# Optimization experiments

Measured on AMD Instinct MI355X. Metric: run time of the kernel, lower is better.

The kernel has to match this reference:

```python
import jax, jax.numpy as jnp
import numpy as np

N = 1048576          # total points
B = 2048             # number of point clouds (segments)
FEAT = 64            # per-point feature dim
ENC = 32             # neighborhood encoder output dim
RADIUS = 1.0


def _linear_params(key, fan_in, fan_out):
    k1, k2 = jax.random.split(key)
    bound = 1.0 / np.sqrt(fan_in)
    w = jax.random.uniform(k1, (fan_in, fan_out), minval=-bound, maxval=bound, dtype=jnp.float32)
    b = jax.random.uniform(k2, (fan_out,), minval=-bound, maxval=bound, dtype=jnp.float32)
    return w, b


def setup_inputs() -> dict:
    key = jax.random.key(0)
    ks = jax.random.split(key, 10)
    points = jax.random.normal(ks[0], (N, 3), dtype=jnp.float32)
    features = jax.random.normal(ks[1], (N, FEAT), dtype=jnp.float32)
    batch = jnp.sort(jax.random.randint(ks[2], (N,), 0, B)).astype(jnp.int64)
    w_ne, b_ne = _linear_params(ks[3], 3, ENC)
    w1, b1 = _linear_params(ks[4], ENC + FEAT, 128)
    w2, b2 = _linear_params(ks[5], 128, 128)
    w3, b3 = _linear_params(ks[6], 128, 128)
    wg1, bg1 = _linear_params(ks[7], 128, 128)
    wg2, bg2 = _linear_params(ks[8], 128, 64)
    wg3, bg3 = _linear_params(ks[9], 64, 32)
    return {"points": points, "features": features, "batch": batch,
            "w_ne": w_ne, "b_ne": b_ne,
            "w1": w1, "b1": b1, "w2": w2, "b2": b2, "w3": w3, "b3": b3,
            "wg1": wg1, "bg1": bg1, "wg2": wg2, "bg2": bg2, "wg3": wg3, "bg3": bg3}


def _segment_max(x, batch, num_segments):
    pooled = jax.ops.segment_max(x, batch, num_segments=num_segments, indices_are_sorted=True)
    # guard empty segments (segment_max fills with -inf)
    return jnp.where(jnp.isneginf(pooled), 0.0, pooled)


def reference(points, features, batch, w_ne, b_ne, w1, b1, w2, b2, w3, b3,
              wg1, bg1, wg2, bg2, wg3, bg3):
    relative_points = points / RADIUS                       # [N, 3]
    # neighborhood encoder: per-point Linear+ReLU, then segment max-pool -> [B, ENC]
    enc = jax.nn.relu(relative_points @ w_ne + b_ne)        # [N, ENC]
    rel_encoded = _segment_max(enc, batch, B)               # [B, ENC]
    rel_enc_mapped = rel_encoded[batch]                     # gather -> [N, ENC]
    fc_input = jnp.concatenate([rel_enc_mapped, features], axis=1)  # [N, ENC+FEAT]
    h = jax.nn.relu(fc_input @ w1 + b1)                     # [N, 128]
    h = jax.nn.relu(h @ w2 + b2)                            # [N, 128]
    h = jax.nn.relu(h @ w3 + b3)                            # [N, 128]
    pooled = _segment_max(h, batch, B)                      # [B, 128]
    g = jax.nn.relu(pooled @ wg1 + bg1)                     # [B, 128]
    g = jax.nn.relu(g @ wg2 + bg2)                          # [B, 64]
    g = jax.nn.relu(g @ wg3 + bg3)                          # [B, 32]
    return g
```

## Files before the change

kernel.cpp:

```cpp
#include <hip/hip_runtime.h>
#include <hip/hip_fp16.h>

#define N_PTS 1048576
#define BSEG  2048
#define XSTR  72

typedef _Float16 half8  __attribute__((ext_vector_type(8)));
typedef _Float16 half4  __attribute__((ext_vector_type(4)));
typedef float    floatx4 __attribute__((ext_vector_type(4)));

__global__ __launch_bounds__(256) void wconv(const float* __restrict__ w1,
                                             const float* __restrict__ w2,
                                             const float* __restrict__ w3,
                                             _Float16* __restrict__ w1T,
                                             _Float16* __restrict__ w2T,
                                             _Float16* __restrict__ w3T) {
    int idx = blockIdx.x * 256 + threadIdx.x;
    if (idx < 8192) {
        int j = idx >> 6, k = idx & 63;
        w1T[idx] = (_Float16)w1[(32 + k) * 128 + j];
    } else if (idx < 8192 + 16384) {
        int i = idx - 8192; int j = i >> 7, k = i & 127;
        w2T[i] = (_Float16)w2[k * 128 + j];
    } else if (idx < 8192 + 32768) {
        int i = idx - 8192 - 16384; int j = i >> 7, k = i & 127;
        w3T[i] = (_Float16)w3[k * 128 + j];
    }
}

__global__ __launch_bounds__(256) void enc_pool(const float* __restrict__ pts,
                                                const int* __restrict__ batch,
                                                const float* __restrict__ wne,
                                                const float* __restrict__ bne,
                                                const float* __restrict__ w1,
                                                const float* __restrict__ b1,
                                                float* __restrict__ b1p) {
    const int b = blockIdx.x, tid = threadIdx.x;
    __shared__ float swne[96];
    __shared__ float sbne[32];
    __shared__ float red[4][32];
    __shared__ float sEnc[32];
    if (tid < 96) swne[tid] = wne[tid];
    if (tid < 32) sbne[tid] = bne[tid];

    int lo = 0, hi = N_PTS;
    while (lo < hi) { int mid = (lo + hi) >> 1; if (batch[mid] < b) lo = mid + 1; else hi = mid; }
    const int start = lo;
    hi = N_PTS;
    while (lo < hi) { int mid = (lo + hi) >> 1; if (batch[mid] < b + 1) lo = mid + 1; else hi = mid; }
    const int end = lo;
    __syncthreads();

    float mx[32];
#pragma unroll
    for (int j = 0; j < 32; j++) mx[j] = 0.f;
    for (int p = start + tid; p < end; p += 256) {
        float x0 = pts[3 * p], x1 = pts[3 * p + 1], x2 = pts[3 * p + 2];
#pragma unroll
        for (int j = 0; j < 32; j++) {
            float e = fmaf(x0, swne[j], fmaf(x1, swne[32 + j], fmaf(x2, swne[64 + j], sbne[j])));
            mx[j] = fmaxf(mx[j], e);
        }
    }
#pragma unroll
    for (int j = 0; j < 32; j++) {
#pragma unroll
        for (int off = 1; off < 64; off <<= 1)
            mx[j] = fmaxf(mx[j], __shfl_xor(mx[j], off, 64));
    }
    const int wv = tid >> 6;
    if ((tid & 63) == 0) {
#pragma unroll
        for (int j = 0; j < 32; j++) red[wv][j] = mx[j];
    }
    __syncthreads();
    if (tid < 32)
        sEnc[tid] = fmaxf(fmaxf(red[0][tid], red[1][tid]), fmaxf(red[2][tid], red[3][tid]));
    __syncthreads();
    if (tid < 128) {
        float acc = b1[tid];
#pragma unroll 8
        for (int k = 0; k < 32; k++) acc = fmaf(sEnc[k], w1[k * 128 + tid], acc);
        b1p[b * 128 + tid] = acc;
    }
}

__global__ __launch_bounds__(256, 3) void fused_mlp(
    const float* __restrict__ feat, const int* __restrict__ batch,
    const float* __restrict__ b1p_g,
    const _Float16* __restrict__ w1T, const _Float16* __restrict__ w2T,
    const _Float16* __restrict__ w3T,
    const float* __restrict__ b2, const float* __restrict__ b3,
    const float* __restrict__ wg1, const float* __restrict__ bg1,
    const float* __restrict__ wg2, const float* __restrict__ bg2,
    const float* __restrict__ wg3, const float* __restrict__ bg3,
    float* __restrict__ out) {
    __shared__ __attribute__((aligned(16))) _Float16 xf[3][16 * XSTR];
    __shared__ __attribute__((aligned(16))) _Float16 h1s[2][16 * 128];
    __shared__ __attribute__((aligned(16))) _Float16 h2s[2][16 * 128];
    __shared__ float pooled[128];
    __shared__ float g1s[128];
    __shared__ float g2s[64];

    const int b = blockIdx.x, tid = threadIdx.x;
    const int lane = tid & 63, jq = tid >> 6;
    const int l15 = lane & 15, quad = lane >> 4;

    int lo = 0, hi = N_PTS;
    while (lo < hi) { int mid = (lo + hi) >> 1; if (batch[mid] < b) lo = mid + 1; else hi = mid; }
    const int start = lo;
    hi = N_PTS;
    while (lo < hi) { int mid = (lo + hi) >> 1; if (batch[mid] < b + 1) lo = mid + 1; else hi = mid; }
    const int end = lo;
    const int n = end - start;
    const int niter = (n + 15) >> 4;

    const int jc0 = jq * 32 + l15, jc1 = jc0 + 16;
    half8 w1f[2][2], w2f[2][4], w3f[2][4];
#pragma unroll
    for (int ks = 0; ks < 2; ks++) {
        w1f[0][ks] = *(const half8*)(w1T + jc0 * 64 + ks * 32 + quad * 8);
        w1f[1][ks] = *(const half8*)(w1T + jc1 * 64 + ks * 32 + quad * 8);
    }
#pragma unroll
    for (int ks = 0; ks < 4; ks++) {
        w2f[0][ks] = *(const half8*)(w2T + jc0 * 128 + ks * 32 + quad * 8);
        w2f[1][ks] = *(const half8*)(w2T + jc1 * 128 + ks * 32 + quad * 8);
        w3f[0][ks] = *(const half8*)(w3T + jc0 * 128 + ks * 32 + quad * 8);
        w3f[1][ks] = *(const half8*)(w3T + jc1 * 128 + ks * 32 + quad * 8);
    }
    float bb1[2], bb2[2], bb3[2];
    bb1[0] = b1p_g[b * 128 + jc0]; bb1[1] = b1p_g[b * 128 + jc1];
    bb2[0] = b2[jc0]; bb2[1] = b2[jc1];
    bb3[0] = b3[jc0]; bb3[1] = b3[jc1];

    const int srow = tid >> 4, scol = tid & 15;
    floatx4 pf;
    auto issue = [&](int it) {
        int p = start + it * 16 + srow;
        if (p < end) pf = *(const floatx4*)(feat + (size_t)p * 64 + scol * 4);
        else         pf = (floatx4){0.f, 0.f, 0.f, 0.f};
    };
    auto commitSlot = [&](int slot) {
        half4 hv = {(_Float16)pf.x, (_Float16)pf.y, (_Float16)pf.z, (_Float16)pf.w};
        *(half4*)(&xf[slot][srow * XSTR + scol * 4]) = hv;
    };
    auto storeH = [&](_Float16* hbuf, floatx4* acc, float* bb) {
#pragma unroll
        for (int jt = 0; jt < 2; jt++) {
            int c = jq * 32 + jt * 16 + l15;
#pragma unroll
            for (int r = 0; r < 4; r++) {
                int rr = quad * 4 + r;
                float v = fmaxf(acc[jt][r] + bb[jt], 0.f);
                hbuf[rr * 128 + ((((c >> 3) ^ rr) & 15) << 3) + (c & 7)] = (_Float16)v;
            }
        }
    };

    if (niter > 0) { issue(0); commitSlot(0); if (niter > 1) issue(1); }
    __syncthreads();

    float vmax[2] = {0.f, 0.f};

    for (int it = 0; it < niter + 2; ++it) {
        const bool doL1 = (it < niter);
        const bool doL2 = (it >= 1) && (it <= niter);
        const bool doL3 = (it >= 2);

        half8 a3[4], a2[4], a1[2];
        if (doL3) {
            const _Float16* src = h2s[(it - 2) & 1];
#pragma unroll
            for (int ks = 0; ks < 4; ks++)
                a3[ks] = *(const half8*)(&src[(l15 << 7) + ((((ks * 4 + quad) ^ l15) & 15) << 3)]);
        }
        if (doL2) {
            const _Float16* src = h1s[(it - 1) & 1];
#pragma unroll
            for (int ks = 0; ks < 4; ks++)
                a2[ks] = *(const half8*)(&src[(l15 << 7) + ((((ks * 4 + quad) ^ l15) & 15) << 3)]);
        }
        if (doL1) {
            const _Float16* src = xf[it % 3];
#pragma unroll
            for (int ks = 0; ks < 2; ks++)
                a1[ks] = *(const half8*)(&src[l15 * XSTR + ks * 32 + quad * 8]);
        }
        if (it + 1 < niter) commitSlot((it + 1) % 3);
        if (it + 2 < niter) issue(it + 2);

        if (doL3) {
            floatx4 acc[2];
            acc[0] = (floatx4){0.f, 0.f, 0.f, 0.f};
            acc[1] = (floatx4){0.f, 0.f, 0.f, 0.f};
#pragma unroll
            for (int ks = 0; ks < 4; ks++) {
                acc[0] = __builtin_amdgcn_mfma_f32_16x16x32_f16(a3[ks], w3f[0][ks], acc[0], 0, 0, 0);
                acc[1] = __builtin_amdgcn_mfma_f32_16x16x32_f16(a3[ks], w3f[1][ks], acc[1], 0, 0, 0);
            }
            const int rowbase = (it - 2) * 16 + quad * 4;
#pragma unroll
            for (int jt = 0; jt < 2; jt++) {
#pragma unroll
                for (int r = 0; r < 4; r++) {
                    float v = ((rowbase + r) < n) ? fmaxf(acc[jt][r] + bb3[jt], 0.f) : 0.f;
                    vmax[jt] = fmaxf(vmax[jt], v);
                }
            }
        }
        if (doL2) {
            floatx4 acc[2];
            acc[0] = (floatx4){0.f, 0.f, 0.f, 0.f};
            acc[1] = (floatx4){0.f, 0.f, 0.f, 0.f};
#pragma unroll
            for (int ks = 0; ks < 4; ks++) {
                acc[0] = __builtin_amdgcn_mfma_f32_16x16x32_f16(a2[ks], w2f[0][ks], acc[0], 0, 0, 0);
                acc[1] = __builtin_amdgcn_mfma_f32_16x16x32_f16(a2[ks], w2f[1][ks], acc[1], 0, 0, 0);
            }
            storeH(h2s[(it - 1) & 1], acc, bb2);
        }
        if (doL1) {
            floatx4 acc[2];
            acc[0] = (floatx4){0.f, 0.f, 0.f, 0.f};
            acc[1] = (floatx4){0.f, 0.f, 0.f, 0.f};
#pragma unroll
            for (int ks = 0; ks < 2; ks++) {
                acc[0] = __builtin_amdgcn_mfma_f32_16x16x32_f16(a1[ks], w1f[0][ks], acc[0], 0, 0, 0);
                acc[1] = __builtin_amdgcn_mfma_f32_16x16x32_f16(a1[ks], w1f[1][ks], acc[1], 0, 0, 0);
            }
            storeH(h1s[it & 1], acc, bb1);
        }
        __syncthreads();
    }

#pragma unroll
    for (int jt = 0; jt < 2; jt++) {
        float m = vmax[jt];
        m = fmaxf(m, __shfl_xor(m, 16, 64));
        m = fmaxf(m, __shfl_xor(m, 32, 64));
        if (quad == 0) pooled[jq * 32 + jt * 16 + l15] = m;
    }
    __syncthreads();

    if (tid < 128) {
        float acc = bg1[tid];
#pragma unroll 8
        for (int k = 0; k < 128; k++) acc = fmaf(pooled[k], wg1[k * 128 + tid], acc);
        g1s[tid] = fmaxf(acc, 0.f);
    }
    __syncthreads();
    if (tid < 64) {
        float acc = bg2[tid];
#pragma unroll 8
        for (int k = 0; k < 128; k++) acc = fmaf(g1s[k], wg2[k * 64 + tid], acc);
        g2s[tid] = fmaxf(acc, 0.f);
    }
    __syncthreads();
    if (tid < 32) {
        float acc = bg3[tid];
#pragma unroll 8
        for (int k = 0; k < 64; k++) acc = fmaf(g2s[k], wg3[k * 32 + tid], acc);
        out[b * 32 + tid] = fmaxf(acc, 0.f);
    }
}

extern "C" void kernel_launch(void* const* d_in, const int* in_sizes, int n_in,
                              void* d_out, int out_size, void* d_ws, size_t ws_size,
                              hipStream_t stream) {
    const float* points = (const float*)d_in[0];
    const float* feat   = (const float*)d_in[1];
    const int*   batch  = (const int*)d_in[2];
    const float* w_ne   = (const float*)d_in[3];
    const float* b_ne   = (const float*)d_in[4];
    const float* w1  = (const float*)d_in[5];
    const float* b1  = (const float*)d_in[6];
    const float* w2  = (const float*)d_in[7];
    const float* b2  = (const float*)d_in[8];
    const float* w3  = (const float*)d_in[9];
    const float* b3  = (const float*)d_in[10];
    const float* wg1 = (const float*)d_in[11];
    const float* bg1 = (const float*)d_in[12];
    const float* wg2 = (const float*)d_in[13];
    const float* bg2 = (const float*)d_in[14];
    const float* wg3 = (const float*)d_in[15];
    const float* bg3 = (const float*)d_in[16];
    float* out = (float*)d_out;

    char* ws = (char*)d_ws;
    float*    b1p = (float*)ws;
    _Float16* w1T = (_Float16*)(ws + 1048576);
    _Float16* w2T = (_Float16*)(ws + 1048576 + 16384);
    _Float16* w3T = (_Float16*)(ws + 1048576 + 16384 + 32768);

    wconv<<<160, 256, 0, stream>>>(w1, w2, w3, w1T, w2T, w3T);
    enc_pool<<<BSEG, 256, 0, stream>>>(points, batch, w_ne, b_ne, w1, b1, b1p);
    fused_mlp<<<BSEG, 256, 0, stream>>>(feat, batch, b1p, w1T, w2T, w3T,
                                        b2, b3, wg1, bg1, wg2, bg2, wg3, bg3, out);
}
```

Baseline: 567.8 us.

## Tile MLP over fixed 256-row blocks with atomic segment-max pooling

The fused MLP stops assigning one block per segment. Each block now takes a fixed 256-point tile and processes 64-row chunks through three MFMA layers. Segment max-pooling goes through integer atomicMax, first into a shared-memory slot table and then into a global pooled buffer; the head MLP moves to a separate kernel. The encoder output is no longer folded into a per-segment bias: it is gathered per row and concatenated as 32 extra K columns of layer 1. The aim is to remove load imbalance from variable segment sizes and the per-block binary search. The cost is a memset, atomics, an extra kernel launch and extra layer-1 work.

```diff
diff --git a/kernel.cpp b/kernel.cpp
--- a/kernel.cpp
+++ b/kernel.cpp
@@ -3,11 +3,13 @@
 
 #define N_PTS 1048576
 #define BSEG  2048
-#define XSTR  72
+#define XSTR  104
+#define NSLOT 8
 
 typedef _Float16 half8  __attribute__((ext_vector_type(8)));
 typedef _Float16 half4  __attribute__((ext_vector_type(4)));
 typedef float    floatx4 __attribute__((ext_vector_type(4)));
+typedef int      intx4   __attribute__((ext_vector_type(4)));
 
 __global__ __launch_bounds__(256) void wconv(const float* __restrict__ w1,
                                              const float* __restrict__ w2,
@@ -16,14 +18,14 @@
                                              _Float16* __restrict__ w2T,
                                              _Float16* __restrict__ w3T) {
     int idx = blockIdx.x * 256 + threadIdx.x;
-    if (idx < 8192) {
-        int j = idx >> 6, k = idx & 63;
-        w1T[idx] = (_Float16)w1[(32 + k) * 128 + j];
-    } else if (idx < 8192 + 16384) {
-        int i = idx - 8192; int j = i >> 7, k = i & 127;
+    if (idx < 12288) {
+        int j = idx / 96, k = idx % 96;
+        w1T[idx] = (_Float16)((k < 64) ? w1[(32 + k) * 128 + j] : w1[(k - 64) * 128 + j]);
+    } else if (idx < 12288 + 16384) {
+        int i = idx - 12288; int j = i >> 7, k = i & 127;
         w2T[i] = (_Float16)w2[k * 128 + j];
-    } else if (idx < 8192 + 32768) {
-        int i = idx - 8192 - 16384; int j = i >> 7, k = i & 127;
+    } else if (idx < 12288 + 32768) {
+        int i = idx - 12288 - 16384; int j = i >> 7, k = i & 127;
         w3T[i] = (_Float16)w3[k * 128 + j];
     }
 }
@@ -32,14 +34,11 @@
                                                 const int* __restrict__ batch,
                                                 const float* __restrict__ wne,
                                                 const float* __restrict__ bne,
-                                                const float* __restrict__ w1,
-                                                const float* __restrict__ b1,
-                                                float* __restrict__ b1p) {
+                                                _Float16* __restrict__ encf) {
     const int b = blockIdx.x, tid = threadIdx.x;
     __shared__ float swne[96];
     __shared__ float sbne[32];
     __shared__ float red[4][32];
-    __shared__ float sEnc[32];
     if (tid < 96) swne[tid] = wne[tid];
     if (tid < 32) sbne[tid] = bne[tid];
 
@@ -74,53 +73,42 @@
         for (int j = 0; j < 32; j++) red[wv][j] = mx[j];
     }
     __syncthreads();
-    if (tid < 32)
-        sEnc[tid] = fmaxf(fmaxf(red[0][tid], red[1][tid]), fmaxf(red[2][tid], red[3][tid]));
-    __syncthreads();
-    if (tid < 128) {
-        float acc = b1[tid];
-#pragma unroll 8
-        for (int k = 0; k < 32; k++) acc = fmaf(sEnc[k], w1[k * 128 + tid], acc);
-        b1p[b * 128 + tid] = acc;
+    if (tid < 32) {
+        float v = fmaxf(fmaxf(red[0][tid], red[1][tid]), fmaxf(red[2][tid], red[3][tid]));
+        encf[b * 32 + tid] = (_Float16)v;
     }
 }
 
 __global__ __launch_bounds__(256, 3) void fused_mlp(
     const float* __restrict__ feat, const int* __restrict__ batch,
-    const float* __restrict__ b1p_g,
+    const _Float16* __restrict__ encf,
     const _Float16* __restrict__ w1T, const _Float16* __restrict__ w2T,
     const _Float16* __restrict__ w3T,
-    const float* __restrict__ b2, const float* __restrict__ b3,
-    const float* __restrict__ wg1, const float* __restrict__ bg1,
-    const float* __restrict__ wg2, const float* __restrict__ bg2,
-    const float* __restrict__ wg3, const float* __restrict__ bg3,
-    float* __restrict__ out) {
-    __shared__ __attribute__((aligned(16))) _Float16 xf[3][16 * XSTR];
-    __shared__ __attribute__((aligned(16))) _Float16 h1s[2][16 * 128];
-    __shared__ __attribute__((aligned(16))) _Float16 h2s[2][16 * 128];
-    __shared__ float pooled[128];
-    __shared__ float g1s[128];
-    __shared__ float g2s[64];
-
-    const int b = blockIdx.x, tid = threadIdx.x;
+    const float* __restrict__ b1, const float* __restrict__ b2,
+    const float* __restrict__ b3,
+    int* __restrict__ pg) {
+    __shared__ __attribute__((aligned(16))) _Float16 xf[64 * XSTR];
+    __shared__ __attribute__((aligned(16))) _Float16 h1s[64 * 128];
+    __shared__ __attribute__((aligned(16))) _Float16 h2s[64 * 128];
+    __shared__ __attribute__((aligned(16))) int sbat[2][64];
+    __shared__ int pooled_s[NSLOT * 128];
+
+    const int tid = threadIdx.x;
     const int lane = tid & 63, jq = tid >> 6;
     const int l15 = lane & 15, quad = lane >> 4;
-
-    int lo = 0, hi = N_PTS;
-    while (lo < hi) { int mid = (lo + hi) >> 1; if (batch[mid] < b) lo = mid + 1; else hi = mid; }
-    const int start = lo;
-    hi = N_PTS;
-    while (lo < hi) { int mid = (lo + hi) >> 1; if (batch[mid] < b + 1) lo = mid + 1; else hi = mid; }
-    const int end = lo;
-    const int n = end - start;
-    const int niter = (n + 15) >> 4;
+    const int rowbase = blockIdx.x << 8;
+    const int seg0 = batch[rowbase];
+    const int segN = batch[rowbase + 255];
+
+#pragma unroll
+    for (int i = 0; i < 4; i++) pooled_s[i * 256 + tid] = 0;
 
     const int jc0 = jq * 32 + l15, jc1 = jc0 + 16;
-    half8 w1f[2][2], w2f[2][4], w3f[2][4];
-#pragma unroll
-    for (int ks = 0; ks < 2; ks++) {
-        w1f[0][ks] = *(const half8*)(w1T + jc0 * 64 + ks * 32 + quad * 8);
-        w1f[1][ks] = *(const half8*)(w1T + jc1 * 64 + ks * 32 + quad * 8);
+    half8 w1f[2][3], w2f[2][4], w3f[2][4];
+#pragma unroll
+    for (int ks = 0; ks < 3; ks++) {
+        w1f[0][ks] = *(const half8*)(w1T + jc0 * 96 + ks * 32 + quad * 8);
+        w1f[1][ks] = *(const half8*)(w1T + jc1 * 96 + ks * 32 + quad * 8);
     }
 #pragma unroll
     for (int ks = 0; ks < 4; ks++) {
@@ -130,22 +118,31 @@
         w3f[1][ks] = *(const half8*)(w3T + jc1 * 128 + ks * 32 + quad * 8);
     }
     float bb1[2], bb2[2], bb3[2];
-    bb1[0] = b1p_g[b * 128 + jc0]; bb1[1] = b1p_g[b * 128 + jc1];
+    bb1[0] = b1[jc0]; bb1[1] = b1[jc1];
     bb2[0] = b2[jc0]; bb2[1] = b2[jc1];
     bb3[0] = b3[jc0]; bb3[1] = b3[jc1];
 
-    const int srow = tid >> 4, scol = tid & 15;
-    floatx4 pf;
-    auto issue = [&](int it) {
-        int p = start + it * 16 + srow;
-        if (p < end) pf = *(const floatx4*)(feat + (size_t)p * 64 + scol * 4);
-        else         pf = (floatx4){0.f, 0.f, 0.f, 0.f};
+    const int srow = tid >> 2, sc4 = tid & 3;
+    floatx4 pf[4]; half8 pe; int pb;
+    auto issue = [&](int p) {
+        const int r = rowbase + p * 64 + srow;
+        pb = batch[r];
+        const float* fr = feat + (size_t)r * 64;
+#pragma unroll
+        for (int i = 0; i < 4; i++) pf[i] = *(const floatx4*)(fr + sc4 * 4 + i * 16);
+        pe = *(const half8*)(encf + pb * 32 + sc4 * 8);
     };
-    auto commitSlot = [&](int slot) {
-        half4 hv = {(_Float16)pf.x, (_Float16)pf.y, (_Float16)pf.z, (_Float16)pf.w};
-        *(half4*)(&xf[slot][srow * XSTR + scol * 4]) = hv;
+    auto commit = [&](int p) {
+        _Float16* xr = &xf[srow * XSTR];
+#pragma unroll
+        for (int i = 0; i < 4; i++) {
+            half4 hv = {(_Float16)pf[i].x, (_Float16)pf[i].y, (_Float16)pf[i].z, (_Float16)pf[i].w};
+            *(half4*)(xr + sc4 * 4 + i * 16) = hv;
+        }
+        *(half8*)(xr + 64 + sc4 * 8) = pe;
+        if (sc4 == 0) sbat[p & 1][srow] = pb;
     };
-    auto storeH = [&](_Float16* hbuf, floatx4* acc, float* bb) {
+    auto storeH = [&](_Float16* hbuf, int mt, floatx4* acc, float* bb) {
 #pragma unroll
         for (int jt = 0; jt < 2; jt++) {
             int c = jq * 32 + jt * 16 + l15;
@@ -153,115 +150,144 @@
             for (int r = 0; r < 4; r++) {
                 int rr = quad * 4 + r;
                 float v = fmaxf(acc[jt][r] + bb[jt], 0.f);
-                hbuf[rr * 128 + ((((c >> 3) ^ rr) & 15) << 3) + (c & 7)] = (_Float16)v;
+                hbuf[(mt * 16 + rr) * 128 + ((((c >> 3) ^ rr) & 15) << 3) + (c & 7)] = (_Float16)v;
             }
         }
     };
 
-    if (niter > 0) { issue(0); commitSlot(0); if (niter > 1) issue(1); }
-    __syncthreads();
-
-    float vmax[2] = {0.f, 0.f};
-
-    for (int it = 0; it < niter + 2; ++it) {
-        const bool doL1 = (it < niter);
-        const bool doL2 = (it >= 1) && (it <= niter);
-        const bool doL3 = (it >= 2);
-
-        half8 a3[4], a2[4], a1[2];
-        if (doL3) {
-            const _Float16* src = h2s[(it - 2) & 1];
-#pragma unroll
-            for (int ks = 0; ks < 4; ks++)
-                a3[ks] = *(const half8*)(&src[(l15 << 7) + ((((ks * 4 + quad) ^ l15) & 15) << 3)]);
-        }
-        if (doL2) {
-            const _Float16* src = h1s[(it - 1) & 1];
-#pragma unroll
-            for (int ks = 0; ks < 4; ks++)
-                a2[ks] = *(const half8*)(&src[(l15 << 7) + ((((ks * 4 + quad) ^ l15) & 15) << 3)]);
-        }
-        if (doL1) {
-            const _Float16* src = xf[it % 3];
-#pragma unroll
-            for (int ks = 0; ks < 2; ks++)
-                a1[ks] = *(const half8*)(&src[l15 * XSTR + ks * 32 + quad * 8]);
-        }
-        if (it + 1 < niter) commitSlot((it + 1) % 3);
-        if (it + 2 < niter) issue(it + 2);
-
-        if (doL3) {
-            floatx4 acc[2];
+    issue(0); commit(0); issue(1);
+    __syncthreads();
+
+    for (int p = 0; p < 4; ++p) {
+        floatx4 acc[2];
+#pragma unroll
+        for (int mt = 0; mt < 4; mt++) {
+            half8 a[3];
+#pragma unroll
+            for (int ks = 0; ks < 3; ks++)
+                a[ks] = *(const half8*)(&xf[(mt * 16 + l15) * XSTR + ks * 32 + quad * 8]);
             acc[0] = (floatx4){0.f, 0.f, 0.f, 0.f};
             acc[1] = (floatx4){0.f, 0.f, 0.f, 0.f};
 #pragma unroll
-            for (int ks = 0; ks < 4; ks++) {
-                acc[0] = __builtin_amdgcn_mfma_f32_16x16x32_f16(a3[ks], w3f[0][ks], acc[0], 0, 0, 0);
-                acc[1] = __builtin_amdgcn_mfma_f32_16x16x32_f16(a3[ks], w3f[1][ks], acc[1], 0, 0, 0);
-            }
-            const int rowbase = (it - 2) * 16 + quad * 4;
-#pragma unroll
-            for (int jt = 0; jt < 2; jt++) {
-#pragma unroll
-                for (int r = 0; r < 4; r++) {
-                    float v = ((rowbase + r) < n) ? fmaxf(acc[jt][r] + bb3[jt], 0.f) : 0.f;
-                    vmax[jt] = fmaxf(vmax[jt], v);
-                }
-            }
-        }
-        if (doL2) {
-            floatx4 acc[2];
+            for (int ks = 0; ks < 3; ks++) {
+                acc[0] = __builtin_amdgcn_mfma_f32_16x16x32_f16(a[ks], w1f[0][ks], acc[0], 0, 0, 0);
+                acc[1] = __builtin_amdgcn_mfma_f32_16x16x32_f16(a[ks], w1f[1][ks], acc[1], 0, 0, 0);
+            }
+            storeH(h1s, mt, acc, bb1);
+        }
+        __syncthreads();
+
+        if (p + 1 < 4) commit(p + 1);
+        if (p + 2 < 4) issue(p + 2);
+
+#pragma unroll
+        for (int mt = 0; mt < 4; mt++) {
+            half8 a[4];
+#pragma unroll
+            for (int ks = 0; ks < 4; ks++)
+                a[ks] = *(const half8*)(&h1s[((mt * 16 + l15) << 7) + ((((ks * 4 + quad) ^ l15) & 15) << 3)]);
             acc[0] = (floatx4){0.f, 0.f, 0.f, 0.f};
             acc[1] = (floatx4){0.f, 0.f, 0.f, 0.f};
 #pragma unroll
             for (int ks = 0; ks < 4; ks++) {
-                acc[0] = __builtin_amdgcn_mfma_f32_16x16x32_f16(a2[ks], w2f[0][ks], acc[0], 0, 0, 0);
-                acc[1] = __builtin_amdgcn_mfma_f32_16x16x32_f16(a2[ks], w2f[1][ks], acc[1], 0, 0, 0);
-            }
-            storeH(h2s[(it - 1) & 1], acc, bb2);
-        }
-        if (doL1) {
-            floatx4 acc[2];
+                acc[0] = __builtin_amdgcn_mfma_f32_16x16x32_f16(a[ks], w2f[0][ks], acc[0], 0, 0, 0);
+                acc[1] = __builtin_amdgcn_mfma_f32_16x16x32_f16(a[ks], w2f[1][ks], acc[1], 0, 0, 0);
+            }
+            storeH(h2s, mt, acc, bb2);
+        }
+        __syncthreads();
+
+#pragma unroll
+        for (int mt = 0; mt < 4; mt++) {
+            half8 a[4];
+#pragma unroll
+            for (int ks = 0; ks < 4; ks++)
+                a[ks] = *(const half8*)(&h2s[((mt * 16 + l15) << 7) + ((((ks * 4 + quad) ^ l15) & 15) << 3)]);
             acc[0] = (floatx4){0.f, 0.f, 0.f, 0.f};
             acc[1] = (floatx4){0.f, 0.f, 0.f, 0.f};
 #pragma unroll
-            for (int ks = 0; ks < 2; ks++) {
-                acc[0] = __builtin_amdgcn_mfma_f32_16x16x32_f16(a1[ks], w1f[0][ks], acc[0], 0, 0, 0);
-                acc[1] = __builtin_amdgcn_mfma_f32_16x16x32_f16(a1[ks], w1f[1][ks], acc[1], 0, 0, 0);
-            }
-            storeH(h1s[it & 1], acc, bb1);
-        }
-        __syncthreads();
-    }
-
-#pragma unroll
-    for (int jt = 0; jt < 2; jt++) {
-        float m = vmax[jt];
-        m = fmaxf(m, __shfl_xor(m, 16, 64));
-        m = fmaxf(m, __shfl_xor(m, 32, 64));
-        if (quad == 0) pooled[jq * 32 + jt * 16 + l15] = m;
-    }
-    __syncthreads();
-
-    if (tid < 128) {
-        float acc = bg1[tid];
+            for (int ks = 0; ks < 4; ks++) {
+                acc[0] = __builtin_amdgcn_mfma_f32_16x16x32_f16(a[ks], w3f[0][ks], acc[0], 0, 0, 0);
+                acc[1] = __builtin_amdgcn_mfma_f32_16x16x32_f16(a[ks], w3f[1][ks], acc[1], 0, 0, 0);
+            }
+            const int sA = sbat[p & 1][mt * 16];
+            const int sB = sbat[p & 1][mt * 16 + 15];
+            if (sA == sB) {
+                const int slot = sA - seg0;
+#pragma unroll
+                for (int jt = 0; jt < 2; jt++) {
+                    float m = fmaxf(fmaxf(fmaxf(acc[jt][0], acc[jt][1]),
+                                          fmaxf(acc[jt][2], acc[jt][3])) + bb3[jt], 0.f);
+                    m = fmaxf(m, __shfl_xor(m, 16, 64));
+                    m = fmaxf(m, __shfl_xor(m, 32, 64));
+                    if (quad == 0) {
+                        int vi = __float_as_int(m);
+                        if (vi) {
+                            int col = jq * 32 + jt * 16 + l15;
+                            if (slot < NSLOT) atomicMax(&pooled_s[slot * 128 + col], vi);
+                            else              atomicMax(&pg[sA * 128 + col], vi);
+                        }
+                    }
+                }
+            } else {
+                intx4 sb4 = *(const intx4*)&sbat[p & 1][mt * 16 + quad * 4];
+#pragma unroll
+                for (int jt = 0; jt < 2; jt++) {
+                    int col = jq * 32 + jt * 16 + l15;
+#pragma unroll
+                    for (int r = 0; r < 4; r++) {
+                        float v = fmaxf(acc[jt][r] + bb3[jt], 0.f);
+                        int vi = __float_as_int(v);
+                        if (vi) {
+                            int sg = sb4[r], slot = sg - seg0;
+                            if (slot < NSLOT) atomicMax(&pooled_s[slot * 128 + col], vi);
+                            else              atomicMax(&pg[sg * 128 + col], vi);
+                        }
+                    }
+                }
+            }
+        }
+    }
+
+    __syncthreads();
+    const int span = segN - seg0 + 1;
+#pragma unroll
+    for (int i = 0; i < 4; i++) {
+        int idx = i * 256 + tid;
+        int slot = idx >> 7, col = idx & 127;
+        if (slot < span) {
+            int v = pooled_s[idx];
+            if (v) atomicMax(&pg[(seg0 + slot) * 128 + col], v);
+        }
+    }
+}
+
+__global__ __launch_bounds__(128) void head(const float* __restrict__ pooled,
+                                            const float* __restrict__ wg1, const float* __restrict__ bg1,
+                                            const float* __restrict__ wg2, const float* __restrict__ bg2,
+                                            const float* __restrict__ wg3, const float* __restrict__ bg3,
+                                            float* __restrict__ out) {
+    const int b = blockIdx.x, tid = threadIdx.x;
+    __shared__ float sp[128], g1[128], g2[64];
+    sp[tid] = pooled[b * 128 + tid];
+    __syncthreads();
+    float a = bg1[tid];
 #pragma unroll 8
-        for (int k = 0; k < 128; k++) acc = fmaf(pooled[k], wg1[k * 128 + tid], acc);
-        g1s[tid] = fmaxf(acc, 0.f);
-    }
+    for (int k = 0; k < 128; k++) a = fmaf(sp[k], wg1[k * 128 + tid], a);
+    g1[tid] = fmaxf(a, 0.f);
     __syncthreads();
     if (tid < 64) {
-        float acc = bg2[tid];
+        float c = bg2[tid];
 #pragma unroll 8
-        for (int k = 0; k < 128; k++) acc = fmaf(g1s[k], wg2[k * 64 + tid], acc);
-        g2s[tid] = fmaxf(acc, 0.f);
+        for (int k = 0; k < 128; k++) c = fmaf(g1[k], wg2[k * 64 + tid], c);
+        g2[tid] = fmaxf(c, 0.f);
     }
     __syncthreads();
     if (tid < 32) {
-        float acc = bg3[tid];
+        float c = bg3[tid];
 #pragma unroll 8
-        for (int k = 0; k < 64; k++) acc = fmaf(g2s[k], wg3[k * 32 + tid], acc);
-        out[b * 32 + tid] = fmaxf(acc, 0.f);
+        for (int k = 0; k < 64; k++) c = fmaf(g2[k], wg3[k * 32 + tid], c);
+        out[b * 32 + tid] = fmaxf(c, 0.f);
     }
 }
 
@@ -288,13 +314,16 @@
     float* out = (float*)d_out;
 
     char* ws = (char*)d_ws;
-    float*    b1p = (float*)ws;
-    _Float16* w1T = (_Float16*)(ws + 1048576);
-    _Float16* w2T = (_Float16*)(ws + 1048576 + 16384);
-    _Float16* w3T = (_Float16*)(ws + 1048576 + 16384 + 32768);
-
-    wconv<<<160, 256, 0, stream>>>(w1, w2, w3, w1T, w2T, w3T);
-    enc_pool<<<BSEG, 256, 0, stream>>>(points, batch, w_ne, b_ne, w1, b1, b1p);
-    fused_mlp<<<BSEG, 256, 0, stream>>>(feat, batch, b1p, w1T, w2T, w3T,
-                                        b2, b3, wg1, bg1, wg2, bg2, wg3, bg3, out);
-}
+    int*      pg   = (int*)ws;
+    _Float16* encf = (_Float16*)(ws + 1048576);
+    _Float16* w1T  = (_Float16*)(ws + 1048576 + 131072);
+    _Float16* w2T  = (_Float16*)(ws + 1048576 + 131072 + 24576);
+    _Float16* w3T  = (_Float16*)(ws + 1048576 + 131072 + 24576 + 32768);
+
+    hipMemsetAsync(pg, 0, BSEG * 128 * sizeof(int), stream);
+    wconv<<<176, 256, 0, stream>>>(w1, w2, w3, w1T, w2T, w3T);
+    enc_pool<<<BSEG, 256, 0, stream>>>(points, batch, w_ne, b_ne, encf);
+    fused_mlp<<<4096, 256, 0, stream>>>(feat, batch, encf, w1T, w2T, w3T,
+                                        b1, b2, b3, pg);
+    head<<<BSEG, 128, 0, stream>>>((const float*)pg, wg1, bg1, wg2, bg2, wg3, bg3, out);
+}
```

Result: no change. 558.1 us (-1.7%).
